# Optimization experiments

Hardware: AMD Instinct MI355X
Metric: run time of the kernel (lower is better)

## Reference

```python
import jax, jax.numpy as jnp
import numpy as np

N_NODES = 50000
N_EDGES = 300000
IN_FEATS = 128
N_HIDDEN = 64
N_HEADS = 4
N_CLASSES = 47
NEG_SLOPE = 0.2


def setup_inputs() -> dict:
    key = jax.random.key(0)
    ks = jax.random.split(key, 16)
    s = 0.1
    inp = {
        "x": jax.random.normal(ks[0], (N_NODES, IN_FEATS), jnp.float32),
        "src": jax.random.randint(ks[1], (N_EDGES,), 0, N_NODES, jnp.int64 if jax.config.jax_enable_x64 else jnp.int32),
        "dst": jax.random.randint(ks[2], (N_EDGES,), 0, N_NODES, jnp.int64 if jax.config.jax_enable_x64 else jnp.int32),
        # layer 1: in_feats -> (heads, hidden)
        "W1": jax.random.normal(ks[3], (IN_FEATS, N_HEADS * N_HIDDEN), jnp.float32) * s,
        "al1": jax.random.normal(ks[4], (N_HEADS, N_HIDDEN), jnp.float32) * s,
        "ar1": jax.random.normal(ks[5], (N_HEADS, N_HIDDEN), jnp.float32) * s,
        "b1": jnp.zeros((N_HEADS * N_HIDDEN,), jnp.float32),
        # layer 2: heads*hidden -> (heads, hidden)
        "W2": jax.random.normal(ks[6], (N_HEADS * N_HIDDEN, N_HEADS * N_HIDDEN), jnp.float32) * s,
        "al2": jax.random.normal(ks[7], (N_HEADS, N_HIDDEN), jnp.float32) * s,
        "ar2": jax.random.normal(ks[8], (N_HEADS, N_HIDDEN), jnp.float32) * s,
        "b2": jnp.zeros((N_HEADS * N_HIDDEN,), jnp.float32),
        # layer 3: heads*hidden -> (1, n_classes)
        "W3": jax.random.normal(ks[9], (N_HEADS * N_HIDDEN, N_CLASSES), jnp.float32) * s,
        "al3": jax.random.normal(ks[10], (1, N_CLASSES), jnp.float32) * s,
        "ar3": jax.random.normal(ks[11], (1, N_CLASSES), jnp.float32) * s,
        "b3": jnp.zeros((N_CLASSES,), jnp.float32),
    }
    return inp


def gat_conv(h, src, dst, W, al, ar, b, n_nodes):
    """DGL GATConv (shared src/dst projection, edge-softmax over dst)."""
    H, D = al.shape
    feat = (h @ W).reshape(n_nodes, H, D)              # [N,H,D]
    el = jnp.sum(feat * al[None], axis=-1)             # [N,H]
    er = jnp.sum(feat * ar[None], axis=-1)             # [N,H]
    e = jax.nn.leaky_relu(el[src] + er[dst], NEG_SLOPE)  # [E,H]
    emax = jax.ops.segment_max(e, dst, num_segments=n_nodes)  # [N,H]
    emax = jnp.where(jnp.isfinite(emax), emax, 0.0)    # empty segments
    ee = jnp.exp(e - emax[dst])                        # [E,H]
    denom = jax.ops.segment_sum(ee, dst, num_segments=n_nodes)  # [N,H]
    alpha = ee / jnp.maximum(denom[dst], 1e-9)         # [E,H]
    msg = feat[src] * alpha[..., None]                 # [E,H,D]
    out = jax.ops.segment_sum(msg, dst, num_segments=n_nodes)   # [N,H,D]
    return out + b.reshape(1, H, D)


def reference(x, src, dst, W1, al1, ar1, b1, W2, al2, ar2, b2, W3, al3, ar3, b3):
    n = x.shape[0]
    h = gat_conv(x, src, dst, W1, al1, ar1, b1, n).reshape(n, -1)  # flatten heads
    h = gat_conv(h, src, dst, W2, al2, ar2, b2, n).reshape(n, -1)
    h = gat_conv(h, src, dst, W3, al3, ar3, b3, n)                 # [N,1,C]
    return h.mean(axis=1)                                          # [N,C]
```

## Files before the change

### kernel.cpp

```cpp
#include <hip/hip_runtime.h>
#include <cstddef>

#define GAT_N 50000
#define GAT_E 300000
#define SCAN_B 256

typedef short bf16x8 __attribute__((ext_vector_type(8)));
typedef float f32x4  __attribute__((ext_vector_type(4)));

__device__ __forceinline__ ushort f2bf(float f) {
    unsigned u = __float_as_uint(f);
    return (ushort)((u + 0x7fffu + ((u >> 16) & 1u)) >> 16);
}
__device__ __forceinline__ float bf2f(ushort h) {
    return __uint_as_float((unsigned)h << 16);
}


__global__ __launch_bounds__(256) void zero_ints(int* __restrict__ a, int n) {
    int i = blockIdx.x * blockDim.x + threadIdx.x;
    int stride = gridDim.x * blockDim.x;
    for (; i < n; i += stride) a[i] = 0;
}

__global__ __launch_bounds__(256) void count_k(
    const int* __restrict__ dst, int* __restrict__ cnt, int E)
{
    int e = blockIdx.x * blockDim.x + threadIdx.x;
    if (e < E) atomicAdd(&cnt[dst[e]], 1);
}

__global__ __launch_bounds__(256) void csr_partial(
    const int* __restrict__ cnt, int* __restrict__ partials, int N, int chunk)
{
    __shared__ int red[256];
    int b = blockIdx.x, t = threadIdx.x;
    int s = 0;
    for (int i = t; i < chunk; i += 256) {
        int idx = b * chunk + i;
        if (idx < N) s += cnt[idx];
    }
    red[t] = s;
    __syncthreads();
    for (int off = 128; off > 0; off >>= 1) {
        if (t < off) red[t] += red[t + off];
        __syncthreads();
    }
    if (t == 0) partials[b] = red[0];
}

__global__ __launch_bounds__(SCAN_B) void csr_scanp(
    int* __restrict__ partials, int* __restrict__ rowptr, int N)
{
    __shared__ int sc[SCAN_B];
    int t = threadIdx.x;
    int v = partials[t];
    sc[t] = v;
    __syncthreads();
    for (int off = 1; off < SCAN_B; off <<= 1) {
        int u = (t >= off) ? sc[t - off] : 0;
        __syncthreads();
        sc[t] += u;
        __syncthreads();
    }
    partials[t] = sc[t] - v;
    if (t == SCAN_B - 1) rowptr[N] = sc[t];
}

__global__ __launch_bounds__(256) void csr_write(
    const int* __restrict__ cnt, const int* __restrict__ partials,
    int* __restrict__ rowptr, int N, int chunk)
{
    __shared__ int sc[256];
    int b = blockIdx.x, t = threadIdx.x;
    int idx = b * chunk + t;
    int v = (t < chunk && idx < N) ? cnt[idx] : 0;
    sc[t] = v;
    __syncthreads();
    for (int off = 1; off < 256; off <<= 1) {
        int u = (t >= off) ? sc[t - off] : 0;
        __syncthreads();
        sc[t] += u;
        __syncthreads();
    }
    if (t < chunk && idx < N) rowptr[idx] = partials[b] + sc[t] - v;
}

__global__ __launch_bounds__(256) void scatter_k(
    const int* __restrict__ src, const int* __restrict__ dst,
    const int* __restrict__ rowptr, int* __restrict__ cursor,
    int* __restrict__ ssrc, int E)
{
    int e = blockIdx.x * blockDim.x + threadIdx.x;
    if (e >= E) return;
    int d = dst[e];
    int p = rowptr[d] + atomicAdd(&cursor[d], 1);
    ssrc[p] = src[e];
}


__global__ __launch_bounds__(256) void convert_x(
    const float* __restrict__ x, ushort* __restrict__ Xh, ushort* __restrict__ Xl,
    long total4)
{
    long i = (long)blockIdx.x * blockDim.x + threadIdx.x;
    long stride = (long)gridDim.x * blockDim.x;
    for (; i < total4; i += stride) {
        float4 v = *(const float4*)(x + i * 4);
        ushort4 h, lo;
        h.x = f2bf(v.x); lo.x = f2bf(v.x - bf2f(h.x));
        h.y = f2bf(v.y); lo.y = f2bf(v.y - bf2f(h.y));
        h.z = f2bf(v.z); lo.z = f2bf(v.z - bf2f(h.z));
        h.w = f2bf(v.w); lo.w = f2bf(v.w - bf2f(h.w));
        *(ushort4*)(Xh + i * 4) = h;
        *(ushort4*)(Xl + i * 4) = lo;
    }
}

__global__ __launch_bounds__(256) void convert_w(
    const float* __restrict__ W, ushort* __restrict__ Wth, ushort* __restrict__ Wtl,
    int K, int M, int Mp)
{
    int idx = blockIdx.x * blockDim.x + threadIdx.x;
    if (idx >= Mp * K) return;
    int c = idx / K, k = idx - c * K;
    float v = (c < M) ? W[(size_t)k * M + c] : 0.f;
    ushort h = f2bf(v);
    Wth[idx] = h;
    Wtl[idx] = f2bf(v - bf2f(h));
}


#define LDK 40

__global__ __launch_bounds__(256) void gemm_feat(
    const ushort* __restrict__ Ah, const ushort* __restrict__ Al,
    const ushort* __restrict__ Wh, const ushort* __restrict__ Wl,
    const float* __restrict__ alw, const float* __restrict__ arw,
    float* __restrict__ feat, float* __restrict__ el, float* __restrict__ er,
    int N, int K, int M, int H, int D)
{
    __shared__ ushort As_h[128 * LDK];
    __shared__ ushort As_l[128 * LDK];
    __shared__ ushort Bs_h[128 * LDK];
    __shared__ ushort Bs_l[128 * LDK];

    const int m0 = blockIdx.x * 128;
    const int n0 = blockIdx.y * 128;
    const int t = threadIdx.x;
    const int w = t >> 6, lane = t & 63;
    const int lr = lane & 15, lg = lane >> 4;
    const int wr = (w >> 1) * 64, wc = (w & 1) * 64;

    f32x4 acc[4][4] = {};

    for (int k0 = 0; k0 < K; k0 += 32) {
        #pragma unroll
        for (int l = 0; l < 2; ++l) {
            int idx = t + l * 256;
            int row = idx >> 2, kk = (idx & 3) * 8;
            bf16x8 vh = {}, vl = {};
            int gr = m0 + row;
            if (gr < N) {
                vh = *(const bf16x8*)(Ah + (size_t)gr * K + k0 + kk);
                vl = *(const bf16x8*)(Al + (size_t)gr * K + k0 + kk);
            }
            bf16x8 wh = *(const bf16x8*)(Wh + (size_t)(n0 + row) * K + k0 + kk);
            bf16x8 wl = *(const bf16x8*)(Wl + (size_t)(n0 + row) * K + k0 + kk);
            *(bf16x8*)&As_h[row * LDK + kk] = vh;
            *(bf16x8*)&As_l[row * LDK + kk] = vl;
            *(bf16x8*)&Bs_h[row * LDK + kk] = wh;
            *(bf16x8*)&Bs_l[row * LDK + kk] = wl;
        }
        __syncthreads();

        bf16x8 a_h[4], a_l[4];
        #pragma unroll
        for (int fi = 0; fi < 4; ++fi) {
            a_h[fi] = *(const bf16x8*)&As_h[(wr + fi * 16 + lr) * LDK + lg * 8];
            a_l[fi] = *(const bf16x8*)&As_l[(wr + fi * 16 + lr) * LDK + lg * 8];
        }
        #pragma unroll
        for (int fj = 0; fj < 4; ++fj) {
            bf16x8 b_h = *(const bf16x8*)&Bs_h[(wc + fj * 16 + lr) * LDK + lg * 8];
            bf16x8 b_l = *(const bf16x8*)&Bs_l[(wc + fj * 16 + lr) * LDK + lg * 8];
            #pragma unroll
            for (int fi = 0; fi < 4; ++fi) {
                acc[fi][fj] = __builtin_amdgcn_mfma_f32_16x16x32_bf16(a_h[fi], b_h, acc[fi][fj], 0, 0, 0);
                acc[fi][fj] = __builtin_amdgcn_mfma_f32_16x16x32_bf16(a_l[fi], b_h, acc[fi][fj], 0, 0, 0);
                acc[fi][fj] = __builtin_amdgcn_mfma_f32_16x16x32_bf16(a_h[fi], b_l, acc[fi][fj], 0, 0, 0);
            }
        }
        __syncthreads();
    }

    #pragma unroll
    for (int fi = 0; fi < 4; ++fi) {
        #pragma unroll
        for (int q = 0; q < 4; ++q) {
            int row = m0 + wr + fi * 16 + 4 * lg + q;
            if (row < N) {
                #pragma unroll
                for (int fj = 0; fj < 4; ++fj) {
                    int col = n0 + wc + fj * 16 + lr;
                    if (col < M) feat[(size_t)row * M + col] = acc[fi][fj][q];
                }
            }
        }
    }

    const int head = (n0 + wc) / D;
    if (head < H) {
        float alv[4], arv[4];
        #pragma unroll
        for (int fj = 0; fj < 4; ++fj) {
            int col = n0 + wc + fj * 16 + lr;
            alv[fj] = (col < M) ? alw[col] : 0.f;
            arv[fj] = (col < M) ? arw[col] : 0.f;
        }
        #pragma unroll
        for (int fi = 0; fi < 4; ++fi) {
            #pragma unroll
            for (int q = 0; q < 4; ++q) {
                float s1 = 0.f, s2 = 0.f;
                #pragma unroll
                for (int fj = 0; fj < 4; ++fj) {
                    s1 = fmaf(acc[fi][fj][q], alv[fj], s1);
                    s2 = fmaf(acc[fi][fj][q], arv[fj], s2);
                }
                #pragma unroll
                for (int mask = 1; mask <= 8; mask <<= 1) {
                    s1 += __shfl_xor(s1, mask);
                    s2 += __shfl_xor(s2, mask);
                }
                int row = m0 + wr + fi * 16 + 4 * lg + q;
                if (lr == 0 && row < N) {
                    el[(size_t)row * H + head] = s1;
                    er[(size_t)row * H + head] = s2;
                }
            }
        }
    }
}


__global__ __launch_bounds__(256) void node_aggr256(
    const int* __restrict__ rowptr, const int* __restrict__ ssrc,
    const float* __restrict__ el, const float* __restrict__ er,
    const float* __restrict__ feat, const float* __restrict__ bias,
    ushort* __restrict__ Ah_out, ushort* __restrict__ Al_out, int N)
{
    int n = blockIdx.x * 4 + (threadIdx.x >> 6);
    if (n >= N) return;
    int lane = threadIdx.x & 63;
    int h = lane >> 4;
    int beg = rowptr[n], end = rowptr[n + 1];
    float erh = er[(size_t)n * 4 + h];

    float m = -__builtin_inff();
    for (int j = beg; j < end; ++j) {
        float sc = el[(size_t)ssrc[j] * 4 + h] + erh;
        sc = sc > 0.f ? sc : 0.2f * sc;
        m = fmaxf(m, sc);
    }

    float denom = 0.f;
    float ax = 0.f, ay = 0.f, az = 0.f, aw = 0.f;
    for (int j = beg; j < end; ++j) {
        int s = ssrc[j];
        float sc = el[(size_t)s * 4 + h] + erh;
        sc = sc > 0.f ? sc : 0.2f * sc;
        float wgt = __expf(sc - m);
        denom += wgt;
        float4 f = *(const float4*)(feat + (size_t)s * 256 + lane * 4);
        ax = fmaf(wgt, f.x, ax);
        ay = fmaf(wgt, f.y, ay);
        az = fmaf(wgt, f.z, az);
        aw = fmaf(wgt, f.w, aw);
    }
    float inv = 1.f / fmaxf(denom, 1e-9f);
    float v0 = fmaf(ax, inv, bias[lane * 4 + 0]);
    float v1 = fmaf(ay, inv, bias[lane * 4 + 1]);
    float v2 = fmaf(az, inv, bias[lane * 4 + 2]);
    float v3 = fmaf(aw, inv, bias[lane * 4 + 3]);
    ushort4 hh, lo;
    hh.x = f2bf(v0); lo.x = f2bf(v0 - bf2f(hh.x));
    hh.y = f2bf(v1); lo.y = f2bf(v1 - bf2f(hh.y));
    hh.z = f2bf(v2); lo.z = f2bf(v2 - bf2f(hh.z));
    hh.w = f2bf(v3); lo.w = f2bf(v3 - bf2f(hh.w));
    *(ushort4*)(Ah_out + (size_t)n * 256 + lane * 4) = hh;
    *(ushort4*)(Al_out + (size_t)n * 256 + lane * 4) = lo;
}

__global__ __launch_bounds__(256) void node_aggr47(
    const int* __restrict__ rowptr, const int* __restrict__ ssrc,
    const float* __restrict__ el, const float* __restrict__ er,
    const float* __restrict__ feat, const float* __restrict__ bias,
    float* __restrict__ out, int N)
{
    int n = blockIdx.x * 4 + (threadIdx.x >> 6);
    if (n >= N) return;
    int lane = threadIdx.x & 63;
    int beg = rowptr[n], end = rowptr[n + 1];
    float erh = er[n];

    float m = -__builtin_inff();
    for (int j = beg; j < end; ++j) {
        float sc = el[ssrc[j]] + erh;
        sc = sc > 0.f ? sc : 0.2f * sc;
        m = fmaxf(m, sc);
    }

    float denom = 0.f, acc = 0.f;
    for (int j = beg; j < end; ++j) {
        int s = ssrc[j];
        float sc = el[s] + erh;
        sc = sc > 0.f ? sc : 0.2f * sc;
        float wgt = __expf(sc - m);
        denom += wgt;
        float f = (lane < 47) ? feat[(size_t)s * 47 + lane] : 0.f;
        acc = fmaf(wgt, f, acc);
    }
    float inv = 1.f / fmaxf(denom, 1e-9f);
    if (lane < 47)
        out[(size_t)n * 47 + lane] = fmaf(acc, inv, bias[lane]);
}


extern "C" void kernel_launch(void* const* d_in, const int* in_sizes, int n_in,
                              void* d_out, int out_size, void* d_ws, size_t ws_size,
                              hipStream_t stream) {
    const float* x   = (const float*)d_in[0];
    const int*   src = (const int*)d_in[1];
    const int*   dst = (const int*)d_in[2];
    const float* W1  = (const float*)d_in[3];
    const float* al1 = (const float*)d_in[4];
    const float* ar1 = (const float*)d_in[5];
    const float* b1  = (const float*)d_in[6];
    const float* W2  = (const float*)d_in[7];
    const float* al2 = (const float*)d_in[8];
    const float* ar2 = (const float*)d_in[9];
    const float* b2  = (const float*)d_in[10];
    const float* W3  = (const float*)d_in[11];
    const float* al3 = (const float*)d_in[12];
    const float* ar3 = (const float*)d_in[13];
    const float* b3  = (const float*)d_in[14];
    float* out = (float*)d_out;

    const int N = GAT_N, E = GAT_E;
    const int chunk = (N + SCAN_B - 1) / SCAN_B;

    char* wsb = (char*)d_ws;
    size_t o = 0;
    float*  feat  = (float*)(wsb + o);  o += (size_t)N * 256 * 4;
    ushort* Ah    = (ushort*)(wsb + o); o += (size_t)N * 256 * 2;
    ushort* Al    = (ushort*)(wsb + o); o += (size_t)N * 256 * 2;
    float*  el    = (float*)(wsb + o);  o += (size_t)N * 4 * 4;
    float*  er    = (float*)(wsb + o);  o += (size_t)N * 4 * 4;
    int* rowptr   = (int*)(wsb + o);    o += (size_t)(N + 1) * 4;
    int* cnt      = (int*)(wsb + o);    o += (size_t)N * 4;
    int* cursor   = (int*)(wsb + o);    o += (size_t)N * 4;
    int* ssrc     = (int*)(wsb + o);    o += (size_t)E * 4;
    int* partials = (int*)(wsb + o);    o += (size_t)SCAN_B * 4;
    ushort* Wt1h  = (ushort*)(wsb + o); o += (size_t)256 * 128 * 2;
    ushort* Wt1l  = (ushort*)(wsb + o); o += (size_t)256 * 128 * 2;
    ushort* Wt2h  = (ushort*)(wsb + o); o += (size_t)256 * 256 * 2;
    ushort* Wt2l  = (ushort*)(wsb + o); o += (size_t)256 * 256 * 2;
    ushort* Wt3h  = (ushort*)(wsb + o); o += (size_t)128 * 256 * 2;
    ushort* Wt3l  = (ushort*)(wsb + o); o += (size_t)128 * 256 * 2;
    ushort* Xh = Ah;
    ushort* Xl = Al;

    dim3 blk(256);
    int gE = (E + 255) / 256;
    int gN = (N + 3) / 4;
    dim3 gemmG((N + 127) / 128, 2);
    dim3 gemmG3((N + 127) / 128, 1);

    zero_ints<<<64, blk, 0, stream>>>(cnt, 2 * N);
    count_k<<<gE, blk, 0, stream>>>(dst, cnt, E);
    csr_partial<<<SCAN_B, blk, 0, stream>>>(cnt, partials, N, chunk);
    csr_scanp<<<1, SCAN_B, 0, stream>>>(partials, rowptr, N);
    csr_write<<<SCAN_B, blk, 0, stream>>>(cnt, partials, rowptr, N, chunk);
    scatter_k<<<gE, blk, 0, stream>>>(src, dst, rowptr, cursor, ssrc, E);

    convert_x<<<2048, blk, 0, stream>>>(x, Xh, Xl, (long)N * 128 / 4);
    convert_w<<<(256 * 128 + 255) / 256, blk, 0, stream>>>(W1, Wt1h, Wt1l, 128, 256, 256);
    convert_w<<<(256 * 256 + 255) / 256, blk, 0, stream>>>(W2, Wt2h, Wt2l, 256, 256, 256);
    convert_w<<<(128 * 256 + 255) / 256, blk, 0, stream>>>(W3, Wt3h, Wt3l, 256, 47, 128);

    gemm_feat<<<gemmG, blk, 0, stream>>>(Xh, Xl, Wt1h, Wt1l, al1, ar1,
                                         feat, el, er, N, 128, 256, 4, 64);
    node_aggr256<<<gN, blk, 0, stream>>>(rowptr, ssrc, el, er, feat, b1, Ah, Al, N);

    gemm_feat<<<gemmG, blk, 0, stream>>>(Ah, Al, Wt2h, Wt2l, al2, ar2,
                                         feat, el, er, N, 256, 256, 4, 64);
    node_aggr256<<<gN, blk, 0, stream>>>(rowptr, ssrc, el, er, feat, b2, Ah, Al, N);

    gemm_feat<<<gemmG3, blk, 0, stream>>>(Ah, Al, Wt3h, Wt3l, al3, ar3,
                                          feat, el, er, N, 256, 47, 1, 47);
    node_aggr47<<<gN, blk, 0, stream>>>(rowptr, ssrc, el, er, feat, b3, out, N);
}
```

Baseline: 351.3 us.

## Precompute per-edge attention scores and split node aggregation across two waves

Adds edge_score kernels that compute leaky-relu(el[src]+er[dst]) once per edge into a contiguous CSR-ordered buffer, with scatter_k now also storing the sorted dst. The aggregation kernels then read scores sequentially instead of re-gathering el twice per edge. node_aggr256 now uses two wavefronts per node, each handling 128 channels, to raise parallelism. The layer-3 feature row stride is padded to 48. This adds extra launches and an E×4 float buffer write and read in exchange for fewer random gathers.

```diff
diff --git a/kernel.cpp b/kernel.cpp
--- a/kernel.cpp
+++ b/kernel.cpp
@@ -89,13 +89,14 @@
 __global__ __launch_bounds__(256) void scatter_k(
     const int* __restrict__ src, const int* __restrict__ dst,
     const int* __restrict__ rowptr, int* __restrict__ cursor,
-    int* __restrict__ ssrc, int E)
+    int* __restrict__ ssrc, int* __restrict__ sdst, int E)
 {
     int e = blockIdx.x * blockDim.x + threadIdx.x;
     if (e >= E) return;
     int d = dst[e];
     int p = rowptr[d] + atomicAdd(&cursor[d], 1);
     ssrc[p] = src[e];
+    sdst[p] = d;
 }
 
 
@@ -138,7 +139,7 @@
     const ushort* __restrict__ Wh, const ushort* __restrict__ Wl,
     const float* __restrict__ alw, const float* __restrict__ arw,
     float* __restrict__ feat, float* __restrict__ el, float* __restrict__ er,
-    int N, int K, int M, int H, int D)
+    int N, int K, int M, int H, int D, int ldF)
 {
     __shared__ ushort As_h[128 * LDK];
     __shared__ ushort As_l[128 * LDK];
@@ -203,7 +204,7 @@
                 #pragma unroll
                 for (int fj = 0; fj < 4; ++fj) {
                     int col = n0 + wc + fj * 16 + lr;
-                    if (col < M) feat[(size_t)row * M + col] = acc[fi][fj][q];
+                    if (col < M) feat[(size_t)row * ldF + col] = acc[fi][fj][q];
                 }
             }
         }
@@ -244,81 +245,95 @@
 }
 
 
+__global__ __launch_bounds__(256) void edge_score4(
+    const int* __restrict__ ssrc, const int* __restrict__ sdst,
+    const float* __restrict__ el, const float* __restrict__ er,
+    float* __restrict__ sc, int E)
+{
+    int p = blockIdx.x * blockDim.x + threadIdx.x;
+    if (p >= E) return;
+    int s = ssrc[p], d = sdst[p];
+    float4 a = *(const float4*)(el + (size_t)s * 4);
+    float4 b = *(const float4*)(er + (size_t)d * 4);
+    float4 v;
+    v.x = a.x + b.x; v.x = v.x > 0.f ? v.x : 0.2f * v.x;
+    v.y = a.y + b.y; v.y = v.y > 0.f ? v.y : 0.2f * v.y;
+    v.z = a.z + b.z; v.z = v.z > 0.f ? v.z : 0.2f * v.z;
+    v.w = a.w + b.w; v.w = v.w > 0.f ? v.w : 0.2f * v.w;
+    *(float4*)(sc + (size_t)p * 4) = v;
+}
+
+__global__ __launch_bounds__(256) void edge_score1(
+    const int* __restrict__ ssrc, const int* __restrict__ sdst,
+    const float* __restrict__ el, const float* __restrict__ er,
+    float* __restrict__ sc, int E)
+{
+    int p = blockIdx.x * blockDim.x + threadIdx.x;
+    if (p >= E) return;
+    float v = el[ssrc[p]] + er[sdst[p]];
+    sc[p] = v > 0.f ? v : 0.2f * v;
+}
+
+
 __global__ __launch_bounds__(256) void node_aggr256(
     const int* __restrict__ rowptr, const int* __restrict__ ssrc,
-    const float* __restrict__ el, const float* __restrict__ er,
-    const float* __restrict__ feat, const float* __restrict__ bias,
+    const float* __restrict__ sc, const float* __restrict__ feat,
+    const float* __restrict__ bias,
     ushort* __restrict__ Ah_out, ushort* __restrict__ Al_out, int N)
 {
-    int n = blockIdx.x * 4 + (threadIdx.x >> 6);
+    int wid = blockIdx.x * 4 + (threadIdx.x >> 6);
+    int n = wid >> 1;
     if (n >= N) return;
+    int half = wid & 1;
     int lane = threadIdx.x & 63;
-    int h = lane >> 4;
+    int c = half * 128 + lane * 2;
+    int h = c >> 6;
     int beg = rowptr[n], end = rowptr[n + 1];
-    float erh = er[(size_t)n * 4 + h];
 
     float m = -__builtin_inff();
+    for (int j = beg; j < end; ++j)
+        m = fmaxf(m, sc[(size_t)j * 4 + h]);
+
+    float denom = 0.f;
+    float a0 = 0.f, a1 = 0.f;
     for (int j = beg; j < end; ++j) {
-        float sc = el[(size_t)ssrc[j] * 4 + h] + erh;
-        sc = sc > 0.f ? sc : 0.2f * sc;
-        m = fmaxf(m, sc);
-    }
-
-    float denom = 0.f;
-    float ax = 0.f, ay = 0.f, az = 0.f, aw = 0.f;
-    for (int j = beg; j < end; ++j) {
+        float wgt = __expf(sc[(size_t)j * 4 + h] - m);
+        denom += wgt;
         int s = ssrc[j];
-        float sc = el[(size_t)s * 4 + h] + erh;
-        sc = sc > 0.f ? sc : 0.2f * sc;
-        float wgt = __expf(sc - m);
-        denom += wgt;
-        float4 f = *(const float4*)(feat + (size_t)s * 256 + lane * 4);
-        ax = fmaf(wgt, f.x, ax);
-        ay = fmaf(wgt, f.y, ay);
-        az = fmaf(wgt, f.z, az);
-        aw = fmaf(wgt, f.w, aw);
+        float2 f = *(const float2*)(feat + (size_t)s * 256 + c);
+        a0 = fmaf(wgt, f.x, a0);
+        a1 = fmaf(wgt, f.y, a1);
     }
     float inv = 1.f / fmaxf(denom, 1e-9f);
-    float v0 = fmaf(ax, inv, bias[lane * 4 + 0]);
-    float v1 = fmaf(ay, inv, bias[lane * 4 + 1]);
-    float v2 = fmaf(az, inv, bias[lane * 4 + 2]);
-    float v3 = fmaf(aw, inv, bias[lane * 4 + 3]);
-    ushort4 hh, lo;
+    float v0 = fmaf(a0, inv, bias[c + 0]);
+    float v1 = fmaf(a1, inv, bias[c + 1]);
+    ushort2 hh, lo;
     hh.x = f2bf(v0); lo.x = f2bf(v0 - bf2f(hh.x));
     hh.y = f2bf(v1); lo.y = f2bf(v1 - bf2f(hh.y));
-    hh.z = f2bf(v2); lo.z = f2bf(v2 - bf2f(hh.z));
-    hh.w = f2bf(v3); lo.w = f2bf(v3 - bf2f(hh.w));
-    *(ushort4*)(Ah_out + (size_t)n * 256 + lane * 4) = hh;
-    *(ushort4*)(Al_out + (size_t)n * 256 + lane * 4) = lo;
+    *(ushort2*)(Ah_out + (size_t)n * 256 + c) = hh;
+    *(ushort2*)(Al_out + (size_t)n * 256 + c) = lo;
 }
 
 __global__ __launch_bounds__(256) void node_aggr47(
     const int* __restrict__ rowptr, const int* __restrict__ ssrc,
-    const float* __restrict__ el, const float* __restrict__ er,
-    const float* __restrict__ feat, const float* __restrict__ bias,
-    float* __restrict__ out, int N)
+    const float* __restrict__ sc, const float* __restrict__ feat,
+    const float* __restrict__ bias, float* __restrict__ out, int N)
 {
     int n = blockIdx.x * 4 + (threadIdx.x >> 6);
     if (n >= N) return;
     int lane = threadIdx.x & 63;
     int beg = rowptr[n], end = rowptr[n + 1];
-    float erh = er[n];
 
     float m = -__builtin_inff();
-    for (int j = beg; j < end; ++j) {
-        float sc = el[ssrc[j]] + erh;
-        sc = sc > 0.f ? sc : 0.2f * sc;
-        m = fmaxf(m, sc);
-    }
+    for (int j = beg; j < end; ++j)
+        m = fmaxf(m, sc[j]);
 
     float denom = 0.f, acc = 0.f;
     for (int j = beg; j < end; ++j) {
+        float wgt = __expf(sc[j] - m);
+        denom += wgt;
         int s = ssrc[j];
-        float sc = el[s] + erh;
-        sc = sc > 0.f ? sc : 0.2f * sc;
-        float wgt = __expf(sc - m);
-        denom += wgt;
-        float f = (lane < 47) ? feat[(size_t)s * 47 + lane] : 0.f;
+        float f = (lane < 47) ? feat[(size_t)s * 48 + lane] : 0.f;
         acc = fmaf(wgt, f, acc);
     }
     float inv = 1.f / fmaxf(denom, 1e-9f);
@@ -361,6 +376,8 @@
     int* cnt      = (int*)(wsb + o);    o += (size_t)N * 4;
     int* cursor   = (int*)(wsb + o);    o += (size_t)N * 4;
     int* ssrc     = (int*)(wsb + o);    o += (size_t)E * 4;
+    int* sdst     = (int*)(wsb + o);    o += (size_t)E * 4;
+    float* scbuf  = (float*)(wsb + o);  o += (size_t)E * 4 * 4;
     int* partials = (int*)(wsb + o);    o += (size_t)SCAN_B * 4;
     ushort* Wt1h  = (ushort*)(wsb + o); o += (size_t)256 * 128 * 2;
     ushort* Wt1l  = (ushort*)(wsb + o); o += (size_t)256 * 128 * 2;
@@ -374,6 +391,7 @@
     dim3 blk(256);
     int gE = (E + 255) / 256;
     int gN = (N + 3) / 4;
+    int gN2 = (2 * N + 3) / 4;
     dim3 gemmG((N + 127) / 128, 2);
     dim3 gemmG3((N + 127) / 128, 1);
 
@@ -382,7 +400,7 @@
     csr_partial<<<SCAN_B, blk, 0, stream>>>(cnt, partials, N, chunk);
     csr_scanp<<<1, SCAN_B, 0, stream>>>(partials, rowptr, N);
     csr_write<<<SCAN_B, blk, 0, stream>>>(cnt, partials, rowptr, N, chunk);
-    scatter_k<<<gE, blk, 0, stream>>>(src, dst, rowptr, cursor, ssrc, E);
+    scatter_k<<<gE, blk, 0, stream>>>(src, dst, rowptr, cursor, ssrc, sdst, E);
 
     convert_x<<<2048, blk, 0, stream>>>(x, Xh, Xl, (long)N * 128 / 4);
     convert_w<<<(256 * 128 + 255) / 256, blk, 0, stream>>>(W1, Wt1h, Wt1l, 128, 256, 256);
@@ -390,14 +408,17 @@
     convert_w<<<(128 * 256 + 255) / 256, blk, 0, stream>>>(W3, Wt3h, Wt3l, 256, 47, 128);
 
     gemm_feat<<<gemmG, blk, 0, stream>>>(Xh, Xl, Wt1h, Wt1l, al1, ar1,
-                                         feat, el, er, N, 128, 256, 4, 64);
-    node_aggr256<<<gN, blk, 0, stream>>>(rowptr, ssrc, el, er, feat, b1, Ah, Al, N);
+                                         feat, el, er, N, 128, 256, 4, 64, 256);
+    edge_score4<<<gE, blk, 0, stream>>>(ssrc, sdst, el, er, scbuf, E);
+    node_aggr256<<<gN2, blk, 0, stream>>>(rowptr, ssrc, scbuf, feat, b1, Ah, Al, N);
 
     gemm_feat<<<gemmG, blk, 0, stream>>>(Ah, Al, Wt2h, Wt2l, al2, ar2,
-                                         feat, el, er, N, 256, 256, 4, 64);
-    node_aggr256<<<gN, blk, 0, stream>>>(rowptr, ssrc, el, er, feat, b2, Ah, Al, N);
+                                         feat, el, er, N, 256, 256, 4, 64, 256);
+    edge_score4<<<gE, blk, 0, stream>>>(ssrc, sdst, el, er, scbuf, E);
+    node_aggr256<<<gN2, blk, 0, stream>>>(rowptr, ssrc, scbuf, feat, b2, Ah, Al, N);
 
     gemm_feat<<<gemmG3, blk, 0, stream>>>(Ah, Al, Wt3h, Wt3l, al3, ar3,
-                                          feat, el, er, N, 256, 47, 1, 47);
-    node_aggr47<<<gN, blk, 0, stream>>>(rowptr, ssrc, el, er, feat, b3, out, N);
-}
+                                          feat, el, er, N, 256, 47, 1, 47, 48);
+    edge_score1<<<gE, blk, 0, stream>>>(ssrc, sdst, el, er, scbuf, E);
+    node_aggr47<<<gN, blk, 0, stream>>>(rowptr, ssrc, scbuf, feat, b3, out, N);
+}
```

After: 404.3 us. 15.1% more time.
